# Optimization experiments

Measured on AMD Instinct MI355X. Metric: run time of the kernel, lower is better.

Reference implementation:

```python
import jax, jax.numpy as jnp
import numpy as np

B, N, D = 32, 1024, 512
NUM_CLASSES = 4
LN_EPS = 1e-5


def _layer_norm(x, g, b):
    mu = jnp.mean(x, axis=-1, keepdims=True)
    var = jnp.mean(jnp.square(x - mu), axis=-1, keepdims=True)
    return (x - mu) * jax.lax.rsqrt(var + LN_EPS) * g + b


def setup_inputs() -> dict:
    key = jax.random.key(0)
    ks = jax.random.split(key, 8)
    s = 0.05
    inp = {
        "sc_matrix": jax.random.uniform(ks[0], (B, N, N), dtype=jnp.float32),
        # GCN encoder params
        "W1": jax.random.normal(ks[1], (N, D), dtype=jnp.float32) * s,
        "b1": jnp.zeros((D,), jnp.float32),
        "W2": jax.random.normal(ks[2], (D, D), dtype=jnp.float32) * s,
        "b2": jnp.zeros((D,), jnp.float32),
        "ln_g": jnp.ones((D,), jnp.float32),
        "ln_b": jnp.zeros((D,), jnp.float32),
        # classifier params
        "Wc1": jax.random.normal(ks[3], (D, 128), dtype=jnp.float32) * s,
        "bc1": jnp.zeros((128,), jnp.float32),
        "g1": jnp.ones((128,), jnp.float32),
        "t1": jnp.zeros((128,), jnp.float32),
        "Wc2": jax.random.normal(ks[4], (128, 64), dtype=jnp.float32) * s,
        "bc2": jnp.zeros((64,), jnp.float32),
        "g2": jnp.ones((64,), jnp.float32),
        "t2": jnp.zeros((64,), jnp.float32),
        "Wc3": jax.random.normal(ks[5], (64, NUM_CLASSES), dtype=jnp.float32) * s,
        "bc3": jnp.zeros((NUM_CLASSES,), jnp.float32),
    }
    return inp


def reference(sc_matrix, W1, b1, W2, b2, ln_g, ln_b,
              Wc1, bc1, g1, t1, Wc2, bc2, g2, t2, Wc3, bc3):
    # Every entry of sc_matrix is nonzero, so the edge list covers all (i,j)
    # pairs incl. self-loops; GCN message passing == dense normalized matmul.
    # PyG gcn_norm: deg[j] = sum_i A[i,j]; out = D^-1/2 A^T D^-1/2 h.
    A = sc_matrix                              # [B,N,N], A[b,i,j] = edge i->j
    deg = jnp.sum(A, axis=-2)                  # col sums, [B,N]
    dis = jnp.where(deg > 0, jax.lax.rsqrt(deg), 0.0)   # deg^{-1/2}
    An = jnp.swapaxes(A, -1, -2) * dis[:, :, None] * dis[:, None, :]  # [B,N,N]

    x = sc_matrix                              # node features = SC rows [B,N,N]
    h = jax.nn.relu(jnp.matmul(An, jnp.matmul(x, W1)) + b1)   # conv1+relu [B,N,D]
    h = jnp.matmul(An, jnp.matmul(h, W2)) + b2                # conv2      [B,N,D]
    z = _layer_norm(h, ln_g, ln_b)

    z_pooled = jnp.mean(z, axis=1)             # [B,D]

    c = jax.nn.relu(_layer_norm(z_pooled @ Wc1 + bc1, g1, t1))
    c = jax.nn.relu(_layer_norm(c @ Wc2 + bc2, g2, t2))
    logits = c @ Wc3 + bc3                     # [B,num_classes]
    return (logits, z_pooled)
```

## Files before the change

### kernel.cpp

```cpp
#include <hip/hip_runtime.h>
#include <hip/hip_bf16.h>

#define B_ 32
#define N_ 1024
#define D_ 512
#define LN_EPS 1e-5f

using bf16 = __bf16;
using bf16x4 = __attribute__((ext_vector_type(4))) __bf16;
using bf16x8 = __attribute__((ext_vector_type(8))) __bf16;
using floatx4 = __attribute__((ext_vector_type(4))) float;

__device__ __forceinline__ void gld16(const bf16* gp, bf16* lp) {
  __builtin_amdgcn_global_load_lds(
      (const __attribute__((address_space(1))) void*)gp,
      (__attribute__((address_space(3))) void*)lp, 16, 0, 0);
}

__global__ __launch_bounds__(256) void k_pre(const float* __restrict__ A,
                                             float* __restrict__ deg_part,
                                             bf16* __restrict__ Abf,
                                             const float* __restrict__ W1,
                                             bf16* __restrict__ W1t,
                                             const float* __restrict__ W2,
                                             bf16* __restrict__ W2t) {
  int blk = blockIdx.x;
  int t = threadIdx.x;
  if (blk < 512) {
    int b = blk >> 4;
    int rc = blk & 15;
    int r0 = rc * 64;
    const float* p = A + (size_t)b * N_ * N_ + (size_t)r0 * N_ + t * 4;
    bf16* op = Abf + (size_t)b * N_ * N_ + (size_t)r0 * N_ + t * 4;
    float4 acc = {0.f, 0.f, 0.f, 0.f};
    #pragma unroll 4
    for (int i = 0; i < 64; ++i) {
      float4 v = *(const float4*)(p + (size_t)i * N_);
      acc.x += v.x; acc.y += v.y; acc.z += v.z; acc.w += v.w;
      bf16x4 o = {(bf16)v.x, (bf16)v.y, (bf16)v.z, (bf16)v.w};
      *(bf16x4*)(op + (size_t)i * N_) = o;
    }
    *(float4*)(deg_part + ((size_t)rc * B_ + b) * N_ + t * 4) = acc;
  } else {
    __shared__ float tile[64][65];
    blk -= 512;
    const float* in; bf16* outp; int R, C, c0, r0;
    if (blk < 128) {
      in = W1; outp = W1t; R = N_; C = D_;
      c0 = (blk & 7) * 64; r0 = (blk >> 3) * 64;
    } else {
      blk -= 128;
      in = W2; outp = W2t; R = D_; C = D_;
      c0 = (blk & 7) * 64; r0 = (blk >> 3) * 64;
    }
    #pragma unroll
    for (int cc = 0; cc < 4; ++cc) {
      int idx = cc * 256 + t;
      int r = idx >> 4, c4 = (idx & 15) << 2;
      const float4 v = *(const float4*)(in + (size_t)(r0 + r) * C + c0 + c4);
      tile[r][c4 + 0] = v.x; tile[r][c4 + 1] = v.y;
      tile[r][c4 + 2] = v.z; tile[r][c4 + 3] = v.w;
    }
    __syncthreads();
    #pragma unroll
    for (int cc = 0; cc < 4; ++cc) {
      int idx = cc * 256 + t;
      int c = idx >> 4, r4 = (idx & 15) << 2;
      bf16* dst = outp + (size_t)(c0 + c) * R + r0 + r4;
      #pragma unroll
      for (int e = 0; e < 4; ++e) dst[e] = (bf16)tile[r4 + e][c];
    }
  }
}

__global__ __launch_bounds__(256) void k_build(const bf16* __restrict__ Abf,
                                               const float* __restrict__ deg_part,
                                               bf16* __restrict__ Anbf) {
  __shared__ float tile[64][65];
  __shared__ float disI[64], disJ[64];
  int b = blockIdx.z;
  int i0 = blockIdx.x * 64;
  int j0 = blockIdx.y * 64;
  int t = threadIdx.x;
  const bf16* Ab = Abf + (size_t)b * N_ * N_;
  bf16* Anb = Anbf + (size_t)b * N_ * N_;
  if (t < 64) {
    float v = 0.f;
    #pragma unroll
    for (int rc = 0; rc < 16; ++rc)
      v += deg_part[((size_t)rc * B_ + b) * N_ + i0 + t];
    disI[t] = v > 0.f ? rsqrtf(v) : 0.f;
  } else if (t < 128) {
    float v = 0.f;
    #pragma unroll
    for (int rc = 0; rc < 16; ++rc)
      v += deg_part[((size_t)rc * B_ + b) * N_ + j0 + (t - 64)];
    disJ[t - 64] = v > 0.f ? rsqrtf(v) : 0.f;
  }
  #pragma unroll
  for (int cc = 0; cc < 2; ++cc) {
    int idx = cc * 256 + t;
    int r = idx >> 3;
    int c8 = (idx & 7) << 3;
    bf16x8 v = *(const bf16x8*)(Ab + (size_t)(j0 + r) * N_ + i0 + c8);
    #pragma unroll
    for (int e = 0; e < 8; ++e) tile[r][c8 + e] = (float)v[e];
  }
  __syncthreads();
  #pragma unroll
  for (int cc = 0; cc < 2; ++cc) {
    int idx = cc * 256 + t;
    int ii = idx >> 3;
    int jj8 = (idx & 7) << 3;
    float di = disI[ii];
    bf16x8 o;
    #pragma unroll
    for (int e = 0; e < 8; ++e)
      o[e] = (bf16)(tile[jj8 + e][ii] * di * disJ[jj8 + e]);
    *(bf16x8*)(Anb + (size_t)(i0 + ii) * N_ + j0 + jj8) = o;
  }
}

template <bool BIAS, bool RELU>
__global__ __launch_bounds__(256, 2) void k_gemm(
    const bf16* __restrict__ Abase, size_t strideA,
    const bf16* __restrict__ Btbase, size_t strideBt,
    bf16* __restrict__ Cbase, size_t strideC,
    const float* __restrict__ bias, int Nn, int K) {
  __shared__ __align__(16) bf16 smem[24576];
  bf16* sA = smem;
  bf16* sB = smem + 8192;
  int nxy = gridDim.x * gridDim.y;
  int L = blockIdx.z * nxy + blockIdx.y * gridDim.x + blockIdx.x;
  int b = (L & 7) + 8 * (L / (nxy * 8));
  int inner = (L >> 3) % nxy;
  int n0 = (inner % gridDim.x) * 256;
  int m0 = (inner / gridDim.x) * 128;

  const bf16* A = Abase + (size_t)b * strideA;
  const bf16* Bt = Btbase + (size_t)b * strideBt;
  int t = threadIdx.x;
  int lane = t & 63, wid = t >> 6;
  int wm = (wid >> 1) * 64, wn = (wid & 1) * 128;
  int l16 = lane & 15, q = lane >> 4;

  int rowoff = lane >> 3;
  int schunk = (lane & 7) ^ rowoff;
  const bf16* agp = A + (size_t)(m0 + wid * 32 + rowoff) * K + schunk * 8;
  const bf16* bgp = Bt + (size_t)(n0 + wid * 64 + rowoff) * K + schunk * 8;
  bf16* alp = &sA[wid * 2048 + lane * 8];
  bf16* blp = &sB[wid * 4096 + lane * 8];

  int xorb = l16 & 7;

  floatx4 acc[4][8];
  #pragma unroll
  for (int i = 0; i < 4; ++i)
    #pragma unroll
    for (int j = 0; j < 8; ++j) acc[i][j] = (floatx4){0.f, 0.f, 0.f, 0.f};

  for (int kt = 0; kt < K; kt += 64) {
    #pragma unroll
    for (int s = 0; s < 4; ++s)
      gld16(agp + (size_t)s * 8 * K + kt, alp + s * 512);
    #pragma unroll
    for (int s = 0; s < 8; ++s)
      gld16(bgp + (size_t)s * 8 * K + kt, blp + s * 512);
    __syncthreads();
    #pragma unroll
    for (int h = 0; h < 2; ++h) {
      int cko = ((q + 4 * h) ^ xorb) * 8;
      bf16x8 af[4], bfr[8];
      #pragma unroll
      for (int mt = 0; mt < 4; ++mt)
        af[mt] = *(const bf16x8*)(&sA[(wm + mt * 16 + l16) * 64 + cko]);
      #pragma unroll
      for (int nt = 0; nt < 8; ++nt)
        bfr[nt] = *(const bf16x8*)(&sB[(wn + nt * 16 + l16) * 64 + cko]);
      #pragma unroll
      for (int mt = 0; mt < 4; ++mt)
        #pragma unroll
        for (int nt = 0; nt < 8; ++nt)
          acc[mt][nt] = __builtin_amdgcn_mfma_f32_16x16x32_bf16(
              af[mt], bfr[nt], acc[mt][nt], 0, 0, 0);
    }
    __syncthreads();
  }

  bf16* C = Cbase + (size_t)b * strideC;
  #pragma unroll
  for (int h = 0; h < 2; ++h) {
    if ((wid >> 1) == h) {
      #pragma unroll
      for (int mt = 0; mt < 4; ++mt)
        #pragma unroll
        for (int nt = 0; nt < 8; ++nt)
          #pragma unroll
          for (int r = 0; r < 4; ++r) {
            float v = acc[mt][nt][r];
            int col = wn + nt * 16 + l16;
            if (BIAS) v += bias[n0 + col];
            if (RELU) v = v > 0.f ? v : 0.f;
            smem[(mt * 16 + q * 4 + r) * 264 + col] = (bf16)v;
          }
    }
    __syncthreads();
    #pragma unroll
    for (int i = 0; i < 8; ++i) {
      int idx = i * 256 + t;
      int row = idx >> 5;
      int c8 = (idx & 31) << 3;
      bf16x8 vv = *(const bf16x8*)(smem + row * 264 + c8);
      *(bf16x8*)(C + (size_t)(m0 + h * 64 + row) * Nn + n0 + c8) = vv;
    }
    if (h == 0) __syncthreads();
  }
}

__global__ __launch_bounds__(256) void k_lnpool(const bf16* __restrict__ H2,
                                                const float* __restrict__ g,
                                                const float* __restrict__ be,
                                                float* __restrict__ zp_part) {
  int b = blockIdx.y;
  int rx = blockIdx.x;
  int r0 = rx * 64;
  int t = threadIdx.x, lane = t & 63, w = t >> 6;
  float ge[8], bee[8];
  #pragma unroll
  for (int e = 0; e < 8; ++e) { ge[e] = g[lane * 8 + e]; bee[e] = be[lane * 8 + e]; }
  float acc[8] = {0, 0, 0, 0, 0, 0, 0, 0};
  for (int rr = 0; rr < 16; ++rr) {
    int row = r0 + w * 16 + rr;
    const bf16* p = H2 + ((size_t)b * N_ + row) * D_ + lane * 8;
    bf16x8 hv = *(const bf16x8*)p;
    float x[8];
    float s = 0.f;
    #pragma unroll
    for (int e = 0; e < 8; ++e) { x[e] = (float)hv[e]; s += x[e]; }
    #pragma unroll
    for (int off = 32; off; off >>= 1) s += __shfl_xor(s, off);
    float mu = s * (1.f / 512.f);
    float ss = 0.f;
    #pragma unroll
    for (int e = 0; e < 8; ++e) { float d = x[e] - mu; ss += d * d; }
    #pragma unroll
    for (int off = 32; off; off >>= 1) ss += __shfl_xor(ss, off);
    float rs = rsqrtf(ss * (1.f / 512.f) + LN_EPS);
    #pragma unroll
    for (int e = 0; e < 8; ++e) acc[e] += (x[e] - mu) * rs * ge[e] + bee[e];
  }
  __shared__ float part[4][512];
  #pragma unroll
  for (int e = 0; e < 8; ++e) part[w][lane * 8 + e] = acc[e];
  __syncthreads();
  #pragma unroll
  for (int k = 0; k < 2; ++k) {
    int d = t + k * 256;
    float s4 = part[0][d] + part[1][d] + part[2][d] + part[3][d];
    zp_part[((size_t)rx * B_ + b) * D_ + d] = s4;
  }
}

__global__ __launch_bounds__(128) void k_cls(
    const float* __restrict__ zp_part,
    const float* __restrict__ Wc1, const float* __restrict__ bc1,
    const float* __restrict__ g1, const float* __restrict__ t1,
    const float* __restrict__ Wc2, const float* __restrict__ bc2,
    const float* __restrict__ g2, const float* __restrict__ t2,
    const float* __restrict__ Wc3, const float* __restrict__ bc3,
    float* __restrict__ out) {
  __shared__ float z[512];
  __shared__ float c1s[128];
  __shared__ float c2s[64];
  __shared__ float red[128];
  int b = blockIdx.x, t = threadIdx.x;
  #pragma unroll
  for (int k = 0; k < 4; ++k) {
    int d = t + k * 128;
    float s = 0.f;
    #pragma unroll
    for (int rx = 0; rx < 16; ++rx)
      s += zp_part[((size_t)rx * B_ + b) * D_ + d];
    float v = s * (1.f / 1024.f);
    z[d] = v;
    out[128 + b * 512 + d] = v;
  }
  __syncthreads();
  float y = bc1[t];
  for (int d = 0; d < 512; ++d) y += z[d] * Wc1[d * 128 + t];
  red[t] = y;
  __syncthreads();
  float mu = 0.f;
  for (int k = 0; k < 128; ++k) mu += red[k];
  mu *= (1.f / 128.f);
  float var = 0.f;
  for (int k = 0; k < 128; ++k) { float dd = red[k] - mu; var += dd * dd; }
  var *= (1.f / 128.f);
  float c = (y - mu) * rsqrtf(var + LN_EPS) * g1[t] + t1[t];
  c1s[t] = c > 0.f ? c : 0.f;
  __syncthreads();
  if (t < 64) {
    float y2 = bc2[t];
    for (int k = 0; k < 128; ++k) y2 += c1s[k] * Wc2[k * 64 + t];
    red[t] = y2;
  }
  __syncthreads();
  if (t < 64) {
    float mu2 = 0.f;
    for (int k = 0; k < 64; ++k) mu2 += red[k];
    mu2 *= (1.f / 64.f);
    float v2 = 0.f;
    for (int k = 0; k < 64; ++k) { float dd = red[k] - mu2; v2 += dd * dd; }
    v2 *= (1.f / 64.f);
    float cc = (red[t] - mu2) * rsqrtf(v2 + LN_EPS) * g2[t] + t2[t];
    c2s[t] = cc > 0.f ? cc : 0.f;
  }
  __syncthreads();
  if (t < 4) {
    float y3 = bc3[t];
    for (int k = 0; k < 64; ++k) y3 += c2s[k] * Wc3[k * 4 + t];
    out[b * 4 + t] = y3;
  }
}

extern "C" void kernel_launch(void* const* d_in, const int* in_sizes, int n_in,
                              void* d_out, int out_size, void* d_ws, size_t ws_size,
                              hipStream_t stream) {
  const float* A   = (const float*)d_in[0];
  const float* W1  = (const float*)d_in[1];
  const float* b1  = (const float*)d_in[2];
  const float* W2  = (const float*)d_in[3];
  const float* b2  = (const float*)d_in[4];
  const float* lng = (const float*)d_in[5];
  const float* lnb = (const float*)d_in[6];
  const float* Wc1 = (const float*)d_in[7];
  const float* bc1 = (const float*)d_in[8];
  const float* g1  = (const float*)d_in[9];
  const float* t1  = (const float*)d_in[10];
  const float* Wc2 = (const float*)d_in[11];
  const float* bc2 = (const float*)d_in[12];
  const float* g2  = (const float*)d_in[13];
  const float* t2  = (const float*)d_in[14];
  const float* Wc3 = (const float*)d_in[15];
  const float* bc3 = (const float*)d_in[16];
  float* out = (float*)d_out;

  char* ws = (char*)d_ws;
  size_t off = 0;
  auto alloc = [&](size_t bytes) {
    char* p = ws + off;
    off += (bytes + 255) & ~(size_t)255;
    return p;
  };
  float* deg_part = (float*)alloc((size_t)16 * B_ * N_ * 4);
  float* zp_part  = (float*)alloc((size_t)16 * B_ * D_ * 4);
  bf16* Anbf  = (bf16*)alloc((size_t)B_ * N_ * N_ * 2);
  bf16* W1t   = (bf16*)alloc((size_t)D_ * N_ * 2);
  bf16* W2t   = (bf16*)alloc((size_t)D_ * D_ * 2);
  bf16* T12t  = (bf16*)alloc((size_t)B_ * D_ * N_ * 2);
  bf16* H1    = (bf16*)alloc((size_t)B_ * N_ * D_ * 2);
  bf16* Abf   = (bf16*)alloc((size_t)B_ * N_ * N_ * 2);
  bf16* H2    = Abf;


  k_pre<<<704, 256, 0, stream>>>(A, deg_part, Abf, W1, W1t, W2, W2t);
  k_build<<<dim3(16, 16, B_), 256, 0, stream>>>(Abf, deg_part, Anbf);

  k_gemm<false, false><<<dim3(4, 4, B_), 256, 0, stream>>>(
      W1t, 0, Abf, (size_t)N_ * N_, T12t, (size_t)D_ * N_, nullptr, N_, N_);
  k_gemm<true, true><<<dim3(2, 8, B_), 256, 0, stream>>>(
      Anbf, (size_t)N_ * N_, T12t, (size_t)D_ * N_, H1, (size_t)N_ * D_, b1, D_, N_);
  k_gemm<false, false><<<dim3(4, 4, B_), 256, 0, stream>>>(
      W2t, 0, H1, (size_t)N_ * D_, T12t, (size_t)D_ * N_, nullptr, N_, D_);
  k_gemm<true, false><<<dim3(2, 8, B_), 256, 0, stream>>>(
      Anbf, (size_t)N_ * N_, T12t, (size_t)D_ * N_, H2, (size_t)N_ * D_, b2, D_, N_);

  k_lnpool<<<dim3(16, B_), 256, 0, stream>>>(H2, lng, lnb, zp_part);
  k_cls<<<B_, 128, 0, stream>>>(zp_part, Wc1, bc1, g1, t1, Wc2, bc2, g2, t2,
                                Wc3, bc3, out);
}
```

Before: 418.4 us.

## Merge first GEMM and normalized-adjacency build into one heterogeneous launch

Combines the W1 GEMM (512 blocks) and the An build/transpose kernel (8192 blocks) into a single launch where block index selects the role. The two are independent, so the memory-bound build blocks can fill CUs alongside compute-bound GEMM blocks and one kernel launch/tail is removed. The build blocks now use the GEMM's 48KB shared allocation and launch_bounds(256,2), which may reduce their occupancy.

```diff
diff --git a/kernel.cpp b/kernel.cpp
--- a/kernel.cpp
+++ b/kernel.cpp
@@ -73,51 +73,142 @@
   }
 }
 
-__global__ __launch_bounds__(256) void k_build(const bf16* __restrict__ Abf,
-                                               const float* __restrict__ deg_part,
-                                               bf16* __restrict__ Anbf) {
-  __shared__ float tile[64][65];
-  __shared__ float disI[64], disJ[64];
-  int b = blockIdx.z;
-  int i0 = blockIdx.x * 64;
-  int j0 = blockIdx.y * 64;
+__global__ __launch_bounds__(256, 2) void k_g1_build(
+    const bf16* __restrict__ W1t, const bf16* __restrict__ Abf,
+    bf16* __restrict__ T12t, const float* __restrict__ deg_part,
+    bf16* __restrict__ Anbf) {
+  __shared__ __align__(16) char smraw[49152];
+  int blk = blockIdx.x;
   int t = threadIdx.x;
-  const bf16* Ab = Abf + (size_t)b * N_ * N_;
-  bf16* Anb = Anbf + (size_t)b * N_ * N_;
-  if (t < 64) {
-    float v = 0.f;
-    #pragma unroll
-    for (int rc = 0; rc < 16; ++rc)
-      v += deg_part[((size_t)rc * B_ + b) * N_ + i0 + t];
-    disI[t] = v > 0.f ? rsqrtf(v) : 0.f;
-  } else if (t < 128) {
-    float v = 0.f;
-    #pragma unroll
-    for (int rc = 0; rc < 16; ++rc)
-      v += deg_part[((size_t)rc * B_ + b) * N_ + j0 + (t - 64)];
-    disJ[t - 64] = v > 0.f ? rsqrtf(v) : 0.f;
-  }
-  #pragma unroll
-  for (int cc = 0; cc < 2; ++cc) {
-    int idx = cc * 256 + t;
-    int r = idx >> 3;
-    int c8 = (idx & 7) << 3;
-    bf16x8 v = *(const bf16x8*)(Ab + (size_t)(j0 + r) * N_ + i0 + c8);
-    #pragma unroll
-    for (int e = 0; e < 8; ++e) tile[r][c8 + e] = (float)v[e];
-  }
-  __syncthreads();
-  #pragma unroll
-  for (int cc = 0; cc < 2; ++cc) {
-    int idx = cc * 256 + t;
-    int ii = idx >> 3;
-    int jj8 = (idx & 7) << 3;
-    float di = disI[ii];
-    bf16x8 o;
-    #pragma unroll
-    for (int e = 0; e < 8; ++e)
-      o[e] = (bf16)(tile[jj8 + e][ii] * di * disJ[jj8 + e]);
-    *(bf16x8*)(Anb + (size_t)(i0 + ii) * N_ + j0 + jj8) = o;
+  if (blk < 512) {
+    bf16* smem = (bf16*)smraw;
+    bf16* sA = smem;
+    bf16* sB = smem + 8192;
+    const int Nn = N_, K = N_;
+    int L = blk;
+    int b = (L & 7) + 8 * (L >> 7);
+    int inner = (L >> 3) & 15;
+    int n0 = (inner & 3) * 256;
+    int m0 = (inner >> 2) * 128;
+
+    const bf16* A = W1t;
+    const bf16* Bt = Abf + (size_t)b * N_ * N_;
+    int lane = t & 63, wid = t >> 6;
+    int wm = (wid >> 1) * 64, wn = (wid & 1) * 128;
+    int l16 = lane & 15, q = lane >> 4;
+    int rowoff = lane >> 3;
+    int schunk = (lane & 7) ^ rowoff;
+    const bf16* agp = A + (size_t)(m0 + wid * 32 + rowoff) * K + schunk * 8;
+    const bf16* bgp = Bt + (size_t)(n0 + wid * 64 + rowoff) * K + schunk * 8;
+    bf16* alp = &sA[wid * 2048 + lane * 8];
+    bf16* blp = &sB[wid * 4096 + lane * 8];
+    int xorb = l16 & 7;
+
+    floatx4 acc[4][8];
+    #pragma unroll
+    for (int i = 0; i < 4; ++i)
+      #pragma unroll
+      for (int j = 0; j < 8; ++j) acc[i][j] = (floatx4){0.f, 0.f, 0.f, 0.f};
+
+    for (int kt = 0; kt < K; kt += 64) {
+      #pragma unroll
+      for (int s = 0; s < 4; ++s)
+        gld16(agp + (size_t)s * 8 * K + kt, alp + s * 512);
+      #pragma unroll
+      for (int s = 0; s < 8; ++s)
+        gld16(bgp + (size_t)s * 8 * K + kt, blp + s * 512);
+      __syncthreads();
+      #pragma unroll
+      for (int h = 0; h < 2; ++h) {
+        int cko = ((q + 4 * h) ^ xorb) * 8;
+        bf16x8 af[4], bfr[8];
+        #pragma unroll
+        for (int mt = 0; mt < 4; ++mt)
+          af[mt] = *(const bf16x8*)(&sA[(wm + mt * 16 + l16) * 64 + cko]);
+        #pragma unroll
+        for (int nt = 0; nt < 8; ++nt)
+          bfr[nt] = *(const bf16x8*)(&sB[(wn + nt * 16 + l16) * 64 + cko]);
+        #pragma unroll
+        for (int mt = 0; mt < 4; ++mt)
+          #pragma unroll
+          for (int nt = 0; nt < 8; ++nt)
+            acc[mt][nt] = __builtin_amdgcn_mfma_f32_16x16x32_bf16(
+                af[mt], bfr[nt], acc[mt][nt], 0, 0, 0);
+      }
+      __syncthreads();
+    }
+
+    bf16* C = T12t + (size_t)b * D_ * N_;
+    #pragma unroll
+    for (int h = 0; h < 2; ++h) {
+      if ((wid >> 1) == h) {
+        #pragma unroll
+        for (int mt = 0; mt < 4; ++mt)
+          #pragma unroll
+          for (int nt = 0; nt < 8; ++nt)
+            #pragma unroll
+            for (int r = 0; r < 4; ++r) {
+              float v = acc[mt][nt][r];
+              int col = wn + nt * 16 + l16;
+              smem[(mt * 16 + q * 4 + r) * 264 + col] = (bf16)v;
+            }
+      }
+      __syncthreads();
+      #pragma unroll
+      for (int i = 0; i < 8; ++i) {
+        int idx = i * 256 + t;
+        int row = idx >> 5;
+        int c8 = (idx & 31) << 3;
+        bf16x8 vv = *(const bf16x8*)(smem + row * 264 + c8);
+        *(bf16x8*)(C + (size_t)(m0 + h * 64 + row) * Nn + n0 + c8) = vv;
+      }
+      if (h == 0) __syncthreads();
+    }
+  } else {
+    float* tile = (float*)smraw;
+    float* disI = (float*)(smraw + 16640);
+    float* disJ = disI + 64;
+    int j2 = blk - 512;
+    int b = j2 >> 8;
+    int i0 = ((j2 >> 4) & 15) * 64;
+    int j0 = (j2 & 15) * 64;
+    const bf16* Ab = Abf + (size_t)b * N_ * N_;
+    bf16* Anb = Anbf + (size_t)b * N_ * N_;
+    if (t < 64) {
+      float v = 0.f;
+      #pragma unroll
+      for (int rc = 0; rc < 16; ++rc)
+        v += deg_part[((size_t)rc * B_ + b) * N_ + i0 + t];
+      disI[t] = v > 0.f ? rsqrtf(v) : 0.f;
+    } else if (t < 128) {
+      float v = 0.f;
+      #pragma unroll
+      for (int rc = 0; rc < 16; ++rc)
+        v += deg_part[((size_t)rc * B_ + b) * N_ + j0 + (t - 64)];
+      disJ[t - 64] = v > 0.f ? rsqrtf(v) : 0.f;
+    }
+    #pragma unroll
+    for (int cc = 0; cc < 2; ++cc) {
+      int idx = cc * 256 + t;
+      int r = idx >> 3;
+      int c8 = (idx & 7) << 3;
+      bf16x8 v = *(const bf16x8*)(Ab + (size_t)(j0 + r) * N_ + i0 + c8);
+      #pragma unroll
+      for (int e = 0; e < 8; ++e) tile[r * 65 + c8 + e] = (float)v[e];
+    }
+    __syncthreads();
+    #pragma unroll
+    for (int cc = 0; cc < 2; ++cc) {
+      int idx = cc * 256 + t;
+      int ii = idx >> 3;
+      int jj8 = (idx & 7) << 3;
+      float di = disI[ii];
+      bf16x8 o;
+      #pragma unroll
+      for (int e = 0; e < 8; ++e)
+        o[e] = (bf16)(tile[(jj8 + e) * 65 + ii] * di * disJ[jj8 + e]);
+      *(bf16x8*)(Anb + (size_t)(i0 + ii) * N_ + j0 + jj8) = o;
+    }
   }
 }
 
@@ -143,14 +234,12 @@
   int lane = t & 63, wid = t >> 6;
   int wm = (wid >> 1) * 64, wn = (wid & 1) * 128;
   int l16 = lane & 15, q = lane >> 4;
-
   int rowoff = lane >> 3;
   int schunk = (lane & 7) ^ rowoff;
   const bf16* agp = A + (size_t)(m0 + wid * 32 + rowoff) * K + schunk * 8;
   const bf16* bgp = Bt + (size_t)(n0 + wid * 64 + rowoff) * K + schunk * 8;
   bf16* alp = &sA[wid * 2048 + lane * 8];
   bf16* blp = &sB[wid * 4096 + lane * 8];
-
   int xorb = l16 & 7;
 
   floatx4 acc[4][8];
@@ -364,10 +453,9 @@
 
 
   k_pre<<<704, 256, 0, stream>>>(A, deg_part, Abf, W1, W1t, W2, W2t);
-  k_build<<<dim3(16, 16, B_), 256, 0, stream>>>(Abf, deg_part, Anbf);
-
-  k_gemm<false, false><<<dim3(4, 4, B_), 256, 0, stream>>>(
-      W1t, 0, Abf, (size_t)N_ * N_, T12t, (size_t)D_ * N_, nullptr, N_, N_);
+
+  k_g1_build<<<8704, 256, 0, stream>>>(W1t, Abf, T12t, deg_part, Anbf);
+
   k_gemm<true, true><<<dim3(2, 8, B_), 256, 0, stream>>>(
       Anbf, (size_t)N_ * N_, T12t, (size_t)D_ * N_, H1, (size_t)N_ * D_, b1, D_, N_);
   k_gemm<false, false><<<dim3(4, 4, B_), 256, 0, stream>>>(
```

Result: no change. 416.3 us (-0.5%).
